# Performance work log

Measured on AMD Instinct MI355X. Metric: run time of the kernel, lower is better.

The kernel has to match this reference:

```python
import jax, jax.numpy as jnp
import numpy as np

N, E, F_IN, F_E, H = 50000, 800000, 128, 16, 64
NEG_SLOPE = 0.2


def _glorot(key, shape):
    fan_in, fan_out = shape[0], shape[-1]
    lim = np.sqrt(6.0 / (fan_in + fan_out))
    return jax.random.uniform(key, shape, jnp.float32, -lim, lim)


def setup_inputs() -> dict:
    key = jax.random.key(0)
    ks = jax.random.split(key, 24)
    inp = {
        "x": jax.random.normal(ks[0], (N, F_IN), jnp.float32),
        "edge_index": jax.random.randint(ks[1], (2, E), 0, N, jnp.int64),
        "edge_attr": jax.random.normal(ks[2], (E, F_E), jnp.float32),
    }
    k = 3
    for i, f_in in zip((1, 2, 3), (F_IN, H, H)):
        inp[f"W{i}"] = _glorot(ks[k], (f_in, H)); k += 1
        inp[f"as{i}"] = _glorot(ks[k], (H,)); k += 1
        inp[f"ad{i}"] = _glorot(ks[k], (H,)); k += 1
        inp[f"We{i}"] = _glorot(ks[k], (F_E, H)); k += 1
        inp[f"ae{i}"] = _glorot(ks[k], (H,)); k += 1
        inp[f"b{i}"] = jnp.zeros((H,), jnp.float32)
        k += 1
    return inp


def gat_conv(x, src, dst, ea, W, a_s, a_d, We, a_e, b):
    # x: [N, f_in]; src/dst: [E'] (self-loops already appended); ea: [E', F_E]
    n = x.shape[0]
    h = x @ W                                   # [N, H]
    alpha_src = h @ a_s                          # [N]
    alpha_dst = h @ a_d                          # [N]
    alpha_e = (ea @ We) @ a_e                    # [E']
    alpha = alpha_src[src] + alpha_dst[dst] + alpha_e
    alpha = jnp.where(alpha > 0, alpha, NEG_SLOPE * alpha)  # leaky_relu
    # segment softmax over incoming edges of each dst node
    amax = jax.ops.segment_max(alpha, dst, num_segments=n)
    ex = jnp.exp(alpha - amax[dst])
    denom = jax.ops.segment_sum(ex, dst, num_segments=n)
    coef = ex / (denom[dst] + 1e-16)             # [E']
    out = jax.ops.segment_sum(h[src] * coef[:, None], dst, num_segments=n)
    return out + b


def reference(x, edge_index, edge_attr,
              W1, as1, ad1, We1, ae1, b1,
              W2, as2, ad2, We2, ae2, b2,
              W3, as3, ad3, We3, ae3, b3):
    n = x.shape[0]
    # add self-loops (PyG GATConv default), edge_attr fill_value='mean'
    loop = jnp.arange(n, dtype=edge_index.dtype)
    src = jnp.concatenate([edge_index[0], loop])
    dst = jnp.concatenate([edge_index[1], loop])
    ea_mean = jnp.mean(edge_attr, axis=0)
    ea = jnp.concatenate([edge_attr, jnp.broadcast_to(ea_mean, (n, edge_attr.shape[1]))], axis=0)

    x1 = jax.nn.elu(gat_conv(x, src, dst, ea, W1, as1, ad1, We1, ae1, b1))
    x2 = jax.nn.elu(gat_conv(x1, src, dst, ea, W2, as2, ad2, We2, ae2, b2))
    x3 = jax.nn.elu(gat_conv(x2, src, dst, ea, W3, as3, ad3, We3, ae3, b3))
    node_embeddings = x1 + x2 + x3
    graph_embedding = jnp.mean(node_embeddings, axis=0, keepdims=True)  # batch=None path
    return node_embeddings, graph_embedding
```

## Files before the change

kernel.cpp:

```cpp
#include <hip/hip_runtime.h>
#include <hip/hip_fp16.h>
#include <math.h>

#define HD 64
#define MAXNBK 256

typedef unsigned long long u64;
typedef _Float16 f16;
typedef _Float16 f16x8 __attribute__((ext_vector_type(8)));
typedef float f32x4 __attribute__((ext_vector_type(4)));

__device__ __forceinline__ u64 pack_rec(int src, float a0, float a1, float a2) {
    return (u64)(src & 0xFFFF)
         | ((u64)__half_as_ushort(__float2half(a0)) << 16)
         | ((u64)__half_as_ushort(__float2half(a1)) << 32)
         | ((u64)__half_as_ushort(__float2half(a2)) << 48);
}

__global__ void k_init(int* cnt, float* gacc, int N) {
    int i = blockIdx.x * blockDim.x + threadIdx.x;
    if (i < N) cnt[i] = 0;
    if (i < HD) gacc[i] = 0.f;
}

__global__ void k_pre(const int* __restrict__ ei, const float* __restrict__ ea,
                      const float* We1, const float* ae1,
                      const float* We2, const float* ae2,
                      const float* We3, const float* ae3,
                      int E, int FE, int* cnt, u64* __restrict__ recE,
                      float* __restrict__ partials) {
    extern __shared__ float lds[];
    float* sEA = lds;
    float* su = sEA + 256 * (FE + 1);
    float* colacc = su + 3 * FE;
    int t = threadIdx.x;
    int ldE = FE + 1;

    if (t < 3 * FE) {
        int l = t / FE, f = t % FE;
        const float* We = (l == 0) ? We1 : (l == 1) ? We2 : We3;
        const float* ae = (l == 0) ? ae1 : (l == 1) ? ae2 : ae3;
        float s = 0.f;
        for (int hh = 0; hh < HD; ++hh) s += We[f * HD + hh] * ae[hh];
        su[t] = s;
    }

    const float4* ea4 = (const float4*)ea;
    size_t tot4 = (size_t)E * FE / 4;
    int per_tile4 = 64 * FE;
    size_t base4 = (size_t)blockIdx.x * per_tile4;
    float4 acc = make_float4(0.f, 0.f, 0.f, 0.f);
    for (int i = t; i < per_tile4; i += 256) {
        size_t g4 = base4 + i;
        if (g4 < tot4) {
            float4 v = ea4[g4];
            acc.x += v.x; acc.y += v.y; acc.z += v.z; acc.w += v.w;
            int g = i * 4;
            int e_loc = g / FE, f = g % FE;
            float* p = &sEA[e_loc * ldE + f];
            p[0] = v.x; p[1] = v.y; p[2] = v.z; p[3] = v.w;
        }
    }
    colacc[t * 4 + 0] = acc.x; colacc[t * 4 + 1] = acc.y;
    colacc[t * 4 + 2] = acc.z; colacc[t * 4 + 3] = acc.w;
    __syncthreads();

    int e = blockIdx.x * 256 + t;
    if (e < E) {
        float a0 = 0.f, a1 = 0.f, a2 = 0.f;
        const float* row = &sEA[t * ldE];
        for (int f = 0; f < FE; ++f) {
            float v = row[f];
            a0 += v * su[f];
            a1 += v * su[FE + f];
            a2 += v * su[2 * FE + f];
        }
        int src = ei[e], dst = ei[E + e];
        recE[e] = pack_rec(src, a0, a1, a2);
        atomicAdd(&cnt[dst], 1);
    }
    if (t < 16) {
        int q = t >> 2, j = t & 3;
        float s = 0.f;
        for (int k = 0; k < 64; ++k) s += colacc[(q + k * 4) * 4 + j];
        partials[blockIdx.x * 16 + (q * 4 + j)] = s;
    }
}

__global__ void k_scanA(const int* __restrict__ cnt, int* pre, int* blocksums, int N) {
    __shared__ int lds[256];
    int t = threadIdx.x;
    int n = blockIdx.x * 256 + t;
    int v = (n < N) ? cnt[n] + 1 : 0;
    lds[t] = v;
    __syncthreads();
    for (int d = 1; d < 256; d <<= 1) {
        int x = (t >= d) ? lds[t - d] : 0;
        __syncthreads();
        lds[t] += x;
        __syncthreads();
    }
    if (n < N) pre[n] = lds[t] - v;
    if (t == 255) blocksums[blockIdx.x] = lds[255];
}

__global__ void k_scanB(int* blocksums, int NBLK, int* total) {
    __shared__ int lds[256];
    int t = threadIdx.x;
    int v = (t < NBLK) ? blocksums[t] : 0;
    lds[t] = v;
    __syncthreads();
    for (int d = 1; d < 256; d <<= 1) {
        int x = (t >= d) ? lds[t - d] : 0;
        __syncthreads();
        lds[t] += x;
        __syncthreads();
    }
    if (t < NBLK) blocksums[t] = lds[t] - v;
    if (t == 255) *total = lds[255];
}

__global__ void k_u2(const float* __restrict__ partials, int NB,
                     const float* We1, const float* ae1,
                     const float* We2, const float* ae2,
                     const float* We3, const float* ae3,
                     float* sE, int FE, float invE,
                     const int* __restrict__ blocksums ,
                     int* bfill , int* bbase, int NBK, int N, int E) {
    __shared__ float red[256 * 4];
    __shared__ float uu[64];
    __shared__ float mea[16];
    int t = threadIdx.x;
    if (t < 3 * FE) {
        int l = t / FE, f = t % FE;
        const float* We = (l == 0) ? We1 : (l == 1) ? We2 : We3;
        const float* ae = (l == 0) ? ae1 : (l == 1) ? ae2 : ae3;
        float s = 0.f;
        for (int hh = 0; hh < HD; ++hh) s += We[f * HD + hh] * ae[hh];
        uu[t] = s;
    }
    const float4* p4 = (const float4*)partials;
    int tot4 = NB * 4;
    float4 acc = make_float4(0.f, 0.f, 0.f, 0.f);
    for (int i = t; i < tot4; i += 256) {
        float4 v = p4[i];
        acc.x += v.x; acc.y += v.y; acc.z += v.z; acc.w += v.w;
    }
    red[t * 4 + 0] = acc.x; red[t * 4 + 1] = acc.y;
    red[t * 4 + 2] = acc.z; red[t * 4 + 3] = acc.w;
    if (t < NBK) {
        int nb_before = min(t * 256, N);
        int base = blocksums[t] - nb_before;
        bbase[t] = base;
        bfill[t * 16] = base;
    }
    if (t == 0) bbase[NBK] = E;
    __syncthreads();
    if (t < 16) {
        int q = t >> 2, j = t & 3;
        float s = 0.f;
        for (int k = 0; k < 64; ++k) s += red[(q + k * 4) * 4 + j];
        mea[q * 4 + j] = s * invE;
    }
    __syncthreads();
    if (t < 3) {
        float a = 0.f;
        for (int f = 0; f < FE; ++f) a += mea[f] * uu[t * FE + f];
        sE[t] = a;
    }
}

__global__ void k_scanC(const int* __restrict__ pre, const int* __restrict__ blocksums,
                        const int* __restrict__ total, int* row_ptr,
                        u64* __restrict__ rec, const float* __restrict__ sE, int N) {
    int n = blockIdx.x * 256 + threadIdx.x;
    if (n < N) {
        int r = pre[n] + blocksums[blockIdx.x];
        row_ptr[n] = r;
        rec[r] = pack_rec(n, sE[0], sE[1], sE[2]);
    }
    if (n == 0) row_ptr[N] = *total;
}

__global__ void k_bucket(const int* __restrict__ ei, const u64* __restrict__ recE,
                         int E, int chunk, int* bfill ,
                         u64* __restrict__ binned, unsigned char* __restrict__ bdstl,
                         int NBK) {
    __shared__ int lcnt[MAXNBK], gb[MAXNBK], lrank[MAXNBK];
    int t = threadIdx.x;
    lcnt[t] = 0;
    __syncthreads();
    int lo = blockIdx.x * chunk, hi = min(E, lo + chunk);
    for (int e = lo + t; e < hi; e += 256)
        atomicAdd(&lcnt[ei[E + e] >> 8], 1);
    __syncthreads();
    if (t < NBK) {
        lrank[t] = 0;
        gb[t] = lcnt[t] ? atomicAdd(&bfill[t * 16], lcnt[t]) : 0;
    }
    __syncthreads();
    for (int e = lo + t; e < hi; e += 256) {
        u64 r = recE[e];
        int dst = ei[E + e];
        int b = dst >> 8;
        int rank = atomicAdd(&lrank[b], 1);
        int pos = gb[b] + rank;
        binned[pos] = r;
        bdstl[pos] = (unsigned char)(dst & 255);
    }
}

__global__ void k_sort(const int* __restrict__ bbase, const int* __restrict__ row_ptr,
                       const u64* __restrict__ binned, const unsigned char* __restrict__ bdstl,
                       u64* __restrict__ rec, int N) {
    __shared__ int lfill[256];
    int b = blockIdx.x, t = threadIdx.x;
    int gnode = (b << 8) + t;
    lfill[t] = (gnode < N) ? row_ptr[gnode] + 1 : 0;
    __syncthreads();
    int base = bbase[b], nrec = bbase[b + 1] - base;
    for (int i = t; i < nrec; i += 256) {
        u64 r = binned[base + i];
        int dl = bdstl[base + i];
        int p = atomicAdd(&lfill[dl], 1);
        rec[p] = r;
    }
}

__global__ void k_gemm(const void* __restrict__ xin, int in_f16,
                       const float* __restrict__ W,
                       const float* __restrict__ a_s, const float* __restrict__ a_d,
                       __half* __restrict__ h, float* __restrict__ as_n,
                       float* __restrict__ ad_n, int N, int K) {
    extern __shared__ char smem[];
    const int SK = K + 8;
    f16* xs = (f16*)smem;
    f16* wt = xs + 64 * SK;
    int t = threadIdx.x;
    int nb = blockIdx.x * 64;

    int nK4 = K >> 2;
    if (in_f16) {
        const __half* xh = (const __half*)xin;
        for (int i = t; i < 64 * nK4; i += 256) {
            int row = i / nK4, c4 = i % nK4;
            int gr = nb + row; if (gr >= N) gr = N - 1;
            u64 v = ((const u64*)(xh + (size_t)gr * K))[c4];
            *(u64*)&xs[row * SK + c4 * 4] = v;
        }
    } else {
        const float* xf = (const float*)xin;
        for (int i = t; i < 64 * nK4; i += 256) {
            int row = i / nK4, c4 = i % nK4;
            int gr = nb + row; if (gr >= N) gr = N - 1;
            float4 v = ((const float4*)(xf + (size_t)gr * K))[c4];
            f16* p = &xs[row * SK + c4 * 4];
            p[0] = (f16)v.x; p[1] = (f16)v.y; p[2] = (f16)v.z; p[3] = (f16)v.w;
        }
    }
    for (int i = t; i < K * 64; i += 256) {
        int k = i >> 6, c = i & 63;
        wt[c * SK + k] = (f16)W[i];
    }
    __syncthreads();

    int wv = t >> 6, lane = t & 63;
    int m = lane & 15, quad = lane >> 4;
    int rowA = wv * 16 + m;

    f32x4 acc[4];
#pragma unroll
    for (int ct = 0; ct < 4; ++ct) acc[ct] = (f32x4){0.f, 0.f, 0.f, 0.f};

    for (int ks = 0; ks < (K >> 5); ++ks) {
        f16x8 a = *(const f16x8*)&xs[rowA * SK + ks * 32 + quad * 8];
#pragma unroll
        for (int ct = 0; ct < 4; ++ct) {
            f16x8 bf = *(const f16x8*)&wt[(ct * 16 + m) * SK + ks * 32 + quad * 8];
            acc[ct] = __builtin_amdgcn_mfma_f32_16x16x32_f16(a, bf, acc[ct], 0, 0, 0);
        }
    }

    __syncthreads();
    f16* ht = xs;
    const int HS = 72;
#pragma unroll
    for (int ct = 0; ct < 4; ++ct)
#pragma unroll
        for (int r = 0; r < 4; ++r) {
            int rl = wv * 16 + quad * 4 + r;
            ht[rl * HS + ct * 16 + m] = (f16)acc[ct][r];
        }
    __syncthreads();

    {
        int row = t >> 2, cb = (t & 3) * 16;
        int gr = nb + row;
        if (gr < N) {
            ulonglong2 v0 = *(const ulonglong2*)&ht[row * HS + cb];
            ulonglong2 v1 = *(const ulonglong2*)&ht[row * HS + cb + 8];
            *(ulonglong2*)(h + (size_t)gr * HD + cb) = v0;
            *(ulonglong2*)(h + (size_t)gr * HD + cb + 8) = v1;
        }
    }
    float ac = a_s[lane], adc = a_d[lane];
    for (int rr = 0; rr < 16; ++rr) {
        int row = wv * 16 + rr, gr = nb + row;
        float v = (float)ht[row * HS + lane];
        float vs = v * ac, vd = v * adc;
#pragma unroll
        for (int dd = 32; dd; dd >>= 1) {
            vs += __shfl_down(vs, dd, 64);
            vd += __shfl_down(vd, dd, 64);
        }
        if (lane == 0 && gr < N) { as_n[gr] = vs; ad_n[gr] = vd; }
    }
}

__global__ void k_aggr(const __half* __restrict__ h, const float* __restrict__ as_n,
                       const float* __restrict__ ad_n, const int* __restrict__ row_ptr,
                       const u64* __restrict__ rec, int l,
                       const float* __restrict__ b, __half* __restrict__ x_out,
                       float* __restrict__ emb, int N, int first) {
    int wave = threadIdx.x >> 6, lane = threadIdx.x & 63;
    int n = blockIdx.x * 4 + wave;
    if (n >= N) return;
    int base = row_ptr[n], end = row_ptr[n + 1];
    float adv = ad_n[n];
    const int shift = 16 * (l + 1);
    float m = -INFINITY, d = 0.f, acc = 0.f;

    for (int c = base; c < end; c += 64) {
        int cnt = min(64, end - c);
        float a = -INFINITY;
        int s = 0;
        if (lane < cnt) {
            u64 r = rec[c + lane];
            s = (int)(r & 0xFFFFull);
            float aE = __half2float(__ushort_as_half((unsigned short)(r >> shift)));
            a = as_n[s] + adv + aE;
            a = (a > 0.f) ? a : 0.2f * a;
        }
        float mc = a;
#pragma unroll
        for (int dd = 32; dd; dd >>= 1) mc = fmaxf(mc, __shfl_xor(mc, dd, 64));
        float mn = fmaxf(m, mc);
        float w = (lane < cnt) ? __expf(a - mn) : 0.f;
        float dc = w;
#pragma unroll
        for (int dd = 32; dd; dd >>= 1) dc += __shfl_xor(dc, dd, 64);
        float sc = __expf(m - mn);
        d = d * sc + dc;
        acc = acc * sc;
        m = mn;
        int j = 0;
        for (; j + 7 < cnt; j += 8) {
            int sx[8]; float wx[8];
#pragma unroll
            for (int q = 0; q < 8; ++q) {
                sx[q] = __shfl(s, j + q, 64);
                wx[q] = __shfl(w, j + q, 64);
            }
            float hx[8];
#pragma unroll
            for (int q = 0; q < 8; ++q)
                hx[q] = __half2float(h[(size_t)sx[q] * HD + lane]);
#pragma unroll
            for (int q = 0; q < 8; ++q) acc += wx[q] * hx[q];
        }
        for (; j + 3 < cnt; j += 4) {
            int s0 = __shfl(s, j, 64), s1 = __shfl(s, j + 1, 64),
                s2 = __shfl(s, j + 2, 64), s3 = __shfl(s, j + 3, 64);
            float w0 = __shfl(w, j, 64), w1 = __shfl(w, j + 1, 64),
                  w2 = __shfl(w, j + 2, 64), w3 = __shfl(w, j + 3, 64);
            float h0 = __half2float(h[(size_t)s0 * HD + lane]);
            float h1 = __half2float(h[(size_t)s1 * HD + lane]);
            float h2 = __half2float(h[(size_t)s2 * HD + lane]);
            float h3 = __half2float(h[(size_t)s3 * HD + lane]);
            acc += w0 * h0; acc += w1 * h1; acc += w2 * h2; acc += w3 * h3;
        }
        for (; j < cnt; ++j) {
            int sj = __shfl(s, j, 64);
            float wj = __shfl(w, j, 64);
            acc += wj * __half2float(h[(size_t)sj * HD + lane]);
        }
    }

    float out = acc / (d + 1e-16f) + b[lane];
    float v = (out > 0.f) ? out : expm1f(out);
    x_out[(size_t)n * HD + lane] = __float2half(v);
    if (first) emb[(size_t)n * HD + lane] = v;
    else emb[(size_t)n * HD + lane] += v;
}

__global__ void k_red(const float* __restrict__ emb, float* gacc, int N) {
    __shared__ float lds[256];
    int f = threadIdx.x & 63, w = threadIdx.x >> 6;
    float s = 0.f;
    for (int n = blockIdx.x * 4 + w; n < N; n += gridDim.x * 4)
        s += emb[(size_t)n * HD + f];
    lds[threadIdx.x] = s;
    __syncthreads();
    if (w == 0) {
        float v = lds[f] + lds[64 + f] + lds[128 + f] + lds[192 + f];
        atomicAdd(&gacc[f], v);
    }
}

__global__ void k_div(const float* __restrict__ gacc, float* out, int N) {
    int f = threadIdx.x;
    if (f < HD) out[(size_t)N * HD + f] = gacc[f] / (float)N;
}

extern "C" void kernel_launch(void* const* d_in, const int* in_sizes, int n_in,
                              void* d_out, int out_size, void* d_ws, size_t ws_size,
                              hipStream_t stream) {
    const float* x = (const float*)d_in[0];
    const int* ei = (const int*)d_in[1];
    const float* ea = (const float*)d_in[2];

    const int FIN = in_sizes[3] / HD;
    const int N = in_sizes[0] / FIN;
    const int E = in_sizes[1] / 2;
    const int FE = in_sizes[2] / E;
    const int Ep = E + N;
    const int NBK = (N + 255) >> 8;
    const int NPRE = 512;

    const float* W[3];  const float* as_[3]; const float* ad_[3];
    const float* We[3]; const float* ae_[3]; const float* bb[3];
    for (int l = 0; l < 3; ++l) {
        W[l]  = (const float*)d_in[3 + 6 * l + 0];
        as_[l] = (const float*)d_in[3 + 6 * l + 1];
        ad_[l] = (const float*)d_in[3 + 6 * l + 2];
        We[l] = (const float*)d_in[3 + 6 * l + 3];
        ae_[l] = (const float*)d_in[3 + 6 * l + 4];
        bb[l] = (const float*)d_in[3 + 6 * l + 5];
    }

    int gN = (N + 255) / 256;
    int ntiles = (E + 255) / 256;
    int chunk = (E + NPRE - 1) / NPRE;

    char* ws = (char*)d_ws;
    size_t off = 0;
    auto alloc = [&](size_t bytes) {
        void* p = ws + off;
        off += (bytes + 255) & ~(size_t)255;
        return p;
    };
    __half* h      = (__half*)alloc((size_t)N * HD * 2);
    __half* x_cur  = (__half*)alloc((size_t)N * HD * 2);
    float*  as_n   = (float*)alloc((size_t)N * 4);
    float*  ad_n   = (float*)alloc((size_t)N * 4);
    int*    cnt    = (int*)alloc((size_t)N * 4);
    int*    rowp   = (int*)alloc((size_t)(N + 1) * 4);
    int*    pre    = (int*)alloc((size_t)N * 4);
    int*    bsums  = (int*)alloc(256 * 4);
    int*    total  = (int*)alloc(4);
    int*    bfill  = (int*)alloc((size_t)MAXNBK * 16 * 4);
    int*    bbase  = (int*)alloc((size_t)(MAXNBK + 1) * 4);
    u64*    rec    = (u64*)alloc((size_t)Ep * 8);
    u64*    recE   = (u64*)alloc((size_t)E * 8);
    u64*    binned = (u64*)alloc((size_t)E * 8);
    unsigned char* bdstl = (unsigned char*)alloc((size_t)E);
    float*  partials = (float*)alloc((size_t)ntiles * 16 * 4);
    float*  sE     = (float*)alloc(3 * 4);
    float*  gacc   = (float*)alloc(HD * 4);
    (void)ws_size; (void)n_in; (void)out_size;

    float* emb = (float*)d_out;

    k_init<<<gN, 256, 0, stream>>>(cnt, gacc, N);
    size_t pre_lds = (size_t)(256 * (FE + 1) + 3 * FE + 256 * 4) * 4;
    k_pre<<<ntiles, 256, pre_lds, stream>>>(ei, ea, We[0], ae_[0], We[1], ae_[1],
                                            We[2], ae_[2], E, FE, cnt, recE, partials);
    k_scanA<<<gN, 256, 0, stream>>>(cnt, pre, bsums, N);
    k_scanB<<<1, 256, 0, stream>>>(bsums, gN, total);
    k_u2<<<1, 256, 0, stream>>>(partials, ntiles, We[0], ae_[0], We[1], ae_[1],
                                We[2], ae_[2], sE, FE, 1.0f / (float)E,
                                bsums, bfill, bbase, NBK, N, E);
    k_scanC<<<gN, 256, 0, stream>>>(pre, bsums, total, rowp, rec, sE, N);
    k_bucket<<<NPRE, 256, 0, stream>>>(ei, recE, E, chunk, bfill, binned, bdstl, NBK);
    k_sort<<<NBK, 256, 0, stream>>>(bbase, rowp, binned, bdstl, rec, N);

    for (int l = 0; l < 3; ++l) {
        const void* xin = (l == 0) ? (const void*)x : (const void*)x_cur;
        int in_f16 = (l == 0) ? 0 : 1;
        int K = (l == 0) ? FIN : HD;
        size_t ldsz = (size_t)(2 * 64 * (K + 8)) * 2;
        k_gemm<<<(N + 63) / 64, 256, ldsz, stream>>>(xin, in_f16, W[l], as_[l], ad_[l],
                                                     h, as_n, ad_n, N, K);
        k_aggr<<<(N + 3) / 4, 256, 0, stream>>>(h, as_n, ad_n, rowp, rec, l,
                                                bb[l], x_cur, emb, N, (l == 0) ? 1 : 0);
    }

    k_red<<<256, 256, 0, stream>>>(emb, gacc, N);
    k_div<<<1, 64, 0, stream>>>(gacc, emb, N);
}
```

Before: 412.2 us.

## Replace per-node degree atomics and global scan with per-bucket counts and in-block scan

Stops doing a global atomicAdd per edge on a per-node count array followed by a three-kernel prefix scan. Instead, a new kernel builds per-bucket (256-node) histograms using shared-memory atomics, the single-block kernel scans the bucket counts, and the sort kernel computes each node's row pointer with a local histogram and scan over its bucket, writing the self-loop records there. This removes the N-sized count, pre and blocksum arrays and two launches, at the cost of reading the destination indices one extra time.

```diff
diff --git a/kernel.cpp b/kernel.cpp
--- a/kernel.cpp
+++ b/kernel.cpp
@@ -17,9 +17,9 @@
          | ((u64)__half_as_ushort(__float2half(a2)) << 48);
 }
 
-__global__ void k_init(int* cnt, float* gacc, int N) {
-    int i = blockIdx.x * blockDim.x + threadIdx.x;
-    if (i < N) cnt[i] = 0;
+__global__ void k_init(int* bcnt, float* gacc, int NBK) {
+    int i = threadIdx.x;
+    if (i < NBK) bcnt[i] = 0;
     if (i < HD) gacc[i] = 0.f;
 }
 
@@ -27,7 +27,7 @@
                       const float* We1, const float* ae1,
                       const float* We2, const float* ae2,
                       const float* We3, const float* ae3,
-                      int E, int FE, int* cnt, u64* __restrict__ recE,
+                      int E, int FE, u64* __restrict__ recE,
                       float* __restrict__ partials) {
     extern __shared__ float lds[];
     float* sEA = lds;
@@ -75,9 +75,8 @@
             a1 += v * su[FE + f];
             a2 += v * su[2 * FE + f];
         }
-        int src = ei[e], dst = ei[E + e];
+        int src = ei[e];
         recE[e] = pack_rec(src, a0, a1, a2);
-        atomicAdd(&cnt[dst], 1);
     }
     if (t < 16) {
         int q = t >> 2, j = t & 3;
@@ -87,37 +86,16 @@
     }
 }
 
-__global__ void k_scanA(const int* __restrict__ cnt, int* pre, int* blocksums, int N) {
-    __shared__ int lds[256];
+__global__ void k_cnt(const int* __restrict__ ei, int E, int chunk, int* bcnt, int NBK) {
+    __shared__ int lc[MAXNBK];
     int t = threadIdx.x;
-    int n = blockIdx.x * 256 + t;
-    int v = (n < N) ? cnt[n] + 1 : 0;
-    lds[t] = v;
-    __syncthreads();
-    for (int d = 1; d < 256; d <<= 1) {
-        int x = (t >= d) ? lds[t - d] : 0;
-        __syncthreads();
-        lds[t] += x;
-        __syncthreads();
-    }
-    if (n < N) pre[n] = lds[t] - v;
-    if (t == 255) blocksums[blockIdx.x] = lds[255];
-}
-
-__global__ void k_scanB(int* blocksums, int NBLK, int* total) {
-    __shared__ int lds[256];
-    int t = threadIdx.x;
-    int v = (t < NBLK) ? blocksums[t] : 0;
-    lds[t] = v;
-    __syncthreads();
-    for (int d = 1; d < 256; d <<= 1) {
-        int x = (t >= d) ? lds[t - d] : 0;
-        __syncthreads();
-        lds[t] += x;
-        __syncthreads();
-    }
-    if (t < NBLK) blocksums[t] = lds[t] - v;
-    if (t == 255) *total = lds[255];
+    lc[t] = 0;
+    __syncthreads();
+    int lo = blockIdx.x * chunk, hi = min(E, lo + chunk);
+    for (int e = lo + t; e < hi; e += 256)
+        atomicAdd(&lc[ei[E + e] >> 8], 1);
+    __syncthreads();
+    if (t < NBK && lc[t]) atomicAdd(&bcnt[t], lc[t]);
 }
 
 __global__ void k_u2(const float* __restrict__ partials, int NB,
@@ -125,11 +103,12 @@
                      const float* We2, const float* ae2,
                      const float* We3, const float* ae3,
                      float* sE, int FE, float invE,
-                     const int* __restrict__ blocksums ,
-                     int* bfill , int* bbase, int NBK, int N, int E) {
+                     const int* __restrict__ bcnt,
+                     int* bfill , int* bbase, int NBK, int E) {
     __shared__ float red[256 * 4];
     __shared__ float uu[64];
     __shared__ float mea[16];
+    __shared__ int ib[256];
     int t = threadIdx.x;
     if (t < 3 * FE) {
         int l = t / FE, f = t % FE;
@@ -148,14 +127,21 @@
     }
     red[t * 4 + 0] = acc.x; red[t * 4 + 1] = acc.y;
     red[t * 4 + 2] = acc.z; red[t * 4 + 3] = acc.w;
+    int v = (t < NBK) ? bcnt[t] : 0;
+    ib[t] = v;
+    __syncthreads();
+    for (int d = 1; d < 256; d <<= 1) {
+        int x = (t >= d) ? ib[t - d] : 0;
+        __syncthreads();
+        ib[t] += x;
+        __syncthreads();
+    }
     if (t < NBK) {
-        int nb_before = min(t * 256, N);
-        int base = blocksums[t] - nb_before;
+        int base = ib[t] - v;
         bbase[t] = base;
         bfill[t * 16] = base;
     }
     if (t == 0) bbase[NBK] = E;
-    __syncthreads();
     if (t < 16) {
         int q = t >> 2, j = t & 3;
         float s = 0.f;
@@ -168,18 +154,6 @@
         for (int f = 0; f < FE; ++f) a += mea[f] * uu[t * FE + f];
         sE[t] = a;
     }
-}
-
-__global__ void k_scanC(const int* __restrict__ pre, const int* __restrict__ blocksums,
-                        const int* __restrict__ total, int* row_ptr,
-                        u64* __restrict__ rec, const float* __restrict__ sE, int N) {
-    int n = blockIdx.x * 256 + threadIdx.x;
-    if (n < N) {
-        int r = pre[n] + blocksums[blockIdx.x];
-        row_ptr[n] = r;
-        rec[r] = pack_rec(n, sE[0], sE[1], sE[2]);
-    }
-    if (n == 0) row_ptr[N] = *total;
 }
 
 __global__ void k_bucket(const int* __restrict__ ei, const u64* __restrict__ recE,
@@ -210,15 +184,35 @@
     }
 }
 
-__global__ void k_sort(const int* __restrict__ bbase, const int* __restrict__ row_ptr,
-                       const u64* __restrict__ binned, const unsigned char* __restrict__ bdstl,
-                       u64* __restrict__ rec, int N) {
-    __shared__ int lfill[256];
+__global__ void k_sort(const int* __restrict__ bbase, const u64* __restrict__ binned,
+                       const unsigned char* __restrict__ bdstl,
+                       const float* __restrict__ sE,
+                       int* __restrict__ row_ptr,
+                       u64* __restrict__ rec, int N, int E) {
+    __shared__ int lcnt[256], lfill[256];
     int b = blockIdx.x, t = threadIdx.x;
+    int base = bbase[b], nrec = bbase[b + 1] - base;
+    lcnt[t] = 0;
+    __syncthreads();
+    for (int i = t; i < nrec; i += 256)
+        atomicAdd(&lcnt[bdstl[base + i]], 1);
+    __syncthreads();
+    int v = lcnt[t];
+    for (int d = 1; d < 256; d <<= 1) {
+        int x = (t >= d) ? lcnt[t - d] : 0;
+        __syncthreads();
+        lcnt[t] += x;
+        __syncthreads();
+    }
     int gnode = (b << 8) + t;
-    lfill[t] = (gnode < N) ? row_ptr[gnode] + 1 : 0;
-    __syncthreads();
-    int base = bbase[b], nrec = bbase[b + 1] - base;
+    int rp = base + gnode + (lcnt[t] - v);
+    if (gnode < N) {
+        row_ptr[gnode] = rp;
+        rec[rp] = pack_rec(gnode, sE[0], sE[1], sE[2]);
+    }
+    if (b == 0 && t == 0) row_ptr[N] = E + N;
+    lfill[t] = rp + 1;
+    __syncthreads();
     for (int i = t; i < nrec; i += 256) {
         u64 r = binned[base + i];
         int dl = bdstl[base + i];
@@ -423,7 +417,6 @@
     const int N = in_sizes[0] / FIN;
     const int E = in_sizes[1] / 2;
     const int FE = in_sizes[2] / E;
-    const int Ep = E + N;
     const int NBK = (N + 255) >> 8;
     const int NPRE = 512;
 
@@ -438,7 +431,6 @@
         bb[l] = (const float*)d_in[3 + 6 * l + 5];
     }
 
-    int gN = (N + 255) / 256;
     int ntiles = (E + 255) / 256;
     int chunk = (E + NPRE - 1) / NPRE;
 
@@ -453,14 +445,11 @@
     __half* x_cur  = (__half*)alloc((size_t)N * HD * 2);
     float*  as_n   = (float*)alloc((size_t)N * 4);
     float*  ad_n   = (float*)alloc((size_t)N * 4);
-    int*    cnt    = (int*)alloc((size_t)N * 4);
     int*    rowp   = (int*)alloc((size_t)(N + 1) * 4);
-    int*    pre    = (int*)alloc((size_t)N * 4);
-    int*    bsums  = (int*)alloc(256 * 4);
-    int*    total  = (int*)alloc(4);
+    int*    bcnt   = (int*)alloc((size_t)MAXNBK * 4);
     int*    bfill  = (int*)alloc((size_t)MAXNBK * 16 * 4);
     int*    bbase  = (int*)alloc((size_t)(MAXNBK + 1) * 4);
-    u64*    rec    = (u64*)alloc((size_t)Ep * 8);
+    u64*    rec    = (u64*)alloc((size_t)(E + N) * 8);
     u64*    recE   = (u64*)alloc((size_t)E * 8);
     u64*    binned = (u64*)alloc((size_t)E * 8);
     unsigned char* bdstl = (unsigned char*)alloc((size_t)E);
@@ -471,18 +460,16 @@
 
     float* emb = (float*)d_out;
 
-    k_init<<<gN, 256, 0, stream>>>(cnt, gacc, N);
+    k_init<<<1, 256, 0, stream>>>(bcnt, gacc, NBK);
     size_t pre_lds = (size_t)(256 * (FE + 1) + 3 * FE + 256 * 4) * 4;
     k_pre<<<ntiles, 256, pre_lds, stream>>>(ei, ea, We[0], ae_[0], We[1], ae_[1],
-                                            We[2], ae_[2], E, FE, cnt, recE, partials);
-    k_scanA<<<gN, 256, 0, stream>>>(cnt, pre, bsums, N);
-    k_scanB<<<1, 256, 0, stream>>>(bsums, gN, total);
+                                            We[2], ae_[2], E, FE, recE, partials);
+    k_cnt<<<NPRE, 256, 0, stream>>>(ei, E, chunk, bcnt, NBK);
     k_u2<<<1, 256, 0, stream>>>(partials, ntiles, We[0], ae_[0], We[1], ae_[1],
                                 We[2], ae_[2], sE, FE, 1.0f / (float)E,
-                                bsums, bfill, bbase, NBK, N, E);
-    k_scanC<<<gN, 256, 0, stream>>>(pre, bsums, total, rowp, rec, sE, N);
+                                bcnt, bfill, bbase, NBK, E);
     k_bucket<<<NPRE, 256, 0, stream>>>(ei, recE, E, chunk, bfill, binned, bdstl, NBK);
-    k_sort<<<NBK, 256, 0, stream>>>(bbase, rowp, binned, bdstl, rec, N);
+    k_sort<<<NBK, 256, 0, stream>>>(bbase, binned, bdstl, sE, rowp, rec, N, E);
 
     for (int l = 0; l < 3; ++l) {
         const void* xin = (l == 0) ? (const void*)x : (const void*)x_cur;
```

After: 396.6 us. 1.04x faster.
